# Kernel optimization log

Measured on AMD Instinct MI355X. Metric: run time of the kernel, lower is better.

## Reference

```python
import jax, jax.numpy as jnp
import numpy as np

HIDDEN = 1024
B, S = 4, 2048

def setup_inputs() -> dict:
    key = jax.random.key(0)
    k1, k2 = jax.random.split(key)
    hidden_states = jax.random.normal(k1, (B, S, HIDDEN), dtype=jnp.float32)
    # torch nn.Linear weight layout: [out_features, in_features]
    W_proj = jax.random.normal(k2, (3 * HIDDEN, HIDDEN), dtype=jnp.float32) * (1.0 / np.sqrt(HIDDEN))
    b_proj = jnp.zeros((3 * HIDDEN,), dtype=jnp.float32)
    return {"hidden_states": hidden_states, "W_proj": W_proj, "b_proj": b_proj}

def reference(hidden_states, W_proj, b_proj):
    h = hidden_states.shape[-1]
    # fused QKV projection: y = x @ W^T + b
    qkv = jnp.einsum('bsh,oh->bso', hidden_states, W_proj) + b_proj
    q, k, v = jnp.split(qkv, 3, axis=-1)  # each [B,S,H]
    scale = 1.0 / jnp.sqrt(jnp.asarray(h, dtype=q.dtype))
    scores = jnp.einsum('bqh,bkh->bqk', q, k) * scale  # [B,S,S]
    attn = jax.nn.softmax(scores, axis=-1)
    out = jnp.einsum('bqk,bkh->bqh', attn, v)
    return out
```

## Files before the change

### kernel.cpp

```cpp
#include <hip/hip_runtime.h>
#include <stdint.h>

#define HIDDEN 1024
#define BATCH  4
#define SEQ    2048
#define TOKENS (BATCH * SEQ)
#define QKVD   (3 * HIDDEN)

typedef unsigned short u16;
typedef __attribute__((ext_vector_type(8))) short   short8;
typedef __attribute__((ext_vector_type(4))) float   floatx4;

__device__ __forceinline__ u16 f32_bf16_rne(float f) {
    unsigned int u = __float_as_uint(f);
    u += 0x7FFFu + ((u >> 16) & 1u);
    return (u16)(u >> 16);
}

#define BAR() asm volatile("s_waitcnt lgkmcnt(0)\n\ts_barrier" ::: "memory")

__global__ __launch_bounds__(256) void cvt_bf16_kernel(
        const float* __restrict__ src, u16* __restrict__ dst, int n4) {
    int i = blockIdx.x * 256 + threadIdx.x;
    if (i >= n4) return;
    float4 v = ((const float4*)src)[i];
    ushort4 o;
    o.x = f32_bf16_rne(v.x); o.y = f32_bf16_rne(v.y);
    o.z = f32_bf16_rne(v.z); o.w = f32_bf16_rne(v.w);
    ((ushort4*)dst)[i] = o;
}

struct Stage { uint4 a0, a1, b0, b1; };

template <int EPI>
__global__ __launch_bounds__(256, 3) void gemm_bt(
        const u16* __restrict__ A, const u16* __restrict__ B,
        void* __restrict__ Cv, const float* __restrict__ bias,
        int K, int lda, int ldb, int ldc,
        size_t sA, size_t sB, size_t sC, float scale) {
    __shared__ u16 As0[4096], As1[4096];
    __shared__ u16 Bs0[4096], Bs1[4096];

    const int t    = threadIdx.x;
    const int lane = t & 63;
    const int wid  = t >> 6;
    const int bm   = blockIdx.y * 128;
    const int bn   = blockIdx.x * 128;

    const u16* Ab = A + (size_t)blockIdx.z * sA;
    const u16* Bb = B + (size_t)blockIdx.z * sB;

    const int srow = lane >> 2;
    const int scol = ((lane & 3) ^ ((lane >> 3) & 3)) * 8;

    const int wm = (wid >> 1) * 64;
    const int wn = (wid & 1) * 64;
    const int fr = lane & 15;
    const int fc = lane >> 4;
    const int foff = fr * 32 + ((fc ^ ((fr >> 1) & 3)) * 8);

    const int c0 = wid * 2, c1 = wid * 2 + 1;
    const u16* gA0 = Ab + (size_t)(bm + c0 * 16 + srow) * lda + scol;
    const u16* gA1 = Ab + (size_t)(bm + c1 * 16 + srow) * lda + scol;
    const u16* gB0 = Bb + (size_t)(bn + c0 * 16 + srow) * ldb + scol;
    const u16* gB1 = Bb + (size_t)(bn + c1 * 16 + srow) * ldb + scol;

    const int nk = K >> 5;

    auto ldst = [&](int kt) -> Stage {
        Stage s;
        const int off = kt << 5;
        s.a0 = *(const uint4*)(gA0 + off);
        s.a1 = *(const uint4*)(gA1 + off);
        s.b0 = *(const uint4*)(gB0 + off);
        s.b1 = *(const uint4*)(gB1 + off);
        return s;
    };
    auto wst = [&](u16* As_, u16* Bs_, const Stage& s) {
        *(uint4*)&As_[c0 * 512 + lane * 8] = s.a0;
        *(uint4*)&As_[c1 * 512 + lane * 8] = s.a1;
        *(uint4*)&Bs_[c0 * 512 + lane * 8] = s.b0;
        *(uint4*)&Bs_[c1 * 512 + lane * 8] = s.b1;
    };

    floatx4 acc[4][4];
#pragma unroll
    for (int i = 0; i < 4; i++)
#pragma unroll
        for (int j = 0; j < 4; j++) acc[i][j] = (floatx4){0.f, 0.f, 0.f, 0.f};

    auto compute = [&](const u16* As_, const u16* Bs_) {
        short8 bfr[4];
#pragma unroll
        for (int ni = 0; ni < 4; ni++)
            bfr[ni] = *(const short8*)&Bs_[((wn >> 4) + ni) * 512 + foff];
#pragma unroll
        for (int mi = 0; mi < 4; mi++) {
            short8 a = *(const short8*)&As_[((wm >> 4) + mi) * 512 + foff];
#pragma unroll
            for (int ni = 0; ni < 4; ni++)
                acc[mi][ni] = __builtin_amdgcn_mfma_f32_16x16x32_bf16(
                    a, bfr[ni], acc[mi][ni], 0, 0, 0);
        }
    };

    Stage ra = ldst(0);
    Stage rb = ldst(nk > 1 ? 1 : 0);
    wst(As0, Bs0, ra);
    BAR();

    for (int kt = 0; kt < nk; kt += 2) {
        ra = ldst(kt + 2 < nk ? kt + 2 : nk - 1);
        compute(As0, Bs0);
        wst(As1, Bs1, rb);
        BAR();
        rb = ldst(kt + 3 < nk ? kt + 3 : nk - 1);
        compute(As1, Bs1);
        wst(As0, Bs0, ra);
        BAR();
    }

    const int crow0 = bm + wm + (lane >> 4) * 4;
    const int ccol0 = bn + wn + fr;
    const size_t coff = (size_t)blockIdx.z * sC;

    if (EPI == 0) {
        u16* C = (u16*)Cv;
        float bv[4];
#pragma unroll
        for (int ni = 0; ni < 4; ni++) bv[ni] = bias[ccol0 + ni * 16];
#pragma unroll
        for (int mi = 0; mi < 4; mi++)
#pragma unroll
            for (int ni = 0; ni < 4; ni++)
#pragma unroll
                for (int r = 0; r < 4; r++)
                    C[coff + (size_t)(crow0 + mi * 16 + r) * ldc + (ccol0 + ni * 16)] =
                        f32_bf16_rne(acc[mi][ni][r] + bv[ni]);
    } else {
        float* C = (float*)Cv;
#pragma unroll
        for (int mi = 0; mi < 4; mi++)
#pragma unroll
            for (int ni = 0; ni < 4; ni++)
#pragma unroll
                for (int r = 0; r < 4; r++) {
                    float v = acc[mi][ni][r];
                    if (EPI == 1) v *= scale;
                    C[coff + (size_t)(crow0 + mi * 16 + r) * ldc + (ccol0 + ni * 16)] = v;
                }
    }
}

__global__ __launch_bounds__(256) void softmax_kernel(
        const float* __restrict__ S, u16* __restrict__ P) {
    __shared__ float redm[4];
    __shared__ float reds[4];
    const size_t base = (size_t)blockIdx.x * SEQ;
    const int t = threadIdx.x, lane = t & 63, wid = t >> 6;
    const float4* src = (const float4*)(S + base);
    float4 a = src[t], b = src[t + 256];

    float m = fmaxf(fmaxf(fmaxf(a.x, a.y), fmaxf(a.z, a.w)),
                    fmaxf(fmaxf(b.x, b.y), fmaxf(b.z, b.w)));
#pragma unroll
    for (int off = 32; off; off >>= 1) m = fmaxf(m, __shfl_xor(m, off, 64));
    if (lane == 0) redm[wid] = m;
    __syncthreads();
    m = fmaxf(fmaxf(redm[0], redm[1]), fmaxf(redm[2], redm[3]));

    float e[8];
    e[0] = __expf(a.x - m); e[1] = __expf(a.y - m);
    e[2] = __expf(a.z - m); e[3] = __expf(a.w - m);
    e[4] = __expf(b.x - m); e[5] = __expf(b.y - m);
    e[6] = __expf(b.z - m); e[7] = __expf(b.w - m);
    float s = e[0] + e[1] + e[2] + e[3] + e[4] + e[5] + e[6] + e[7];
#pragma unroll
    for (int off = 32; off; off >>= 1) s += __shfl_xor(s, off, 64);
    if (lane == 0) reds[wid] = s;
    __syncthreads();
    s = reds[0] + reds[1] + reds[2] + reds[3];
    const float r = 1.f / s;

    ushort4* dst = (ushort4*)(P + base);
    ushort4 o0, o1;
    o0.x = f32_bf16_rne(e[0] * r); o0.y = f32_bf16_rne(e[1] * r);
    o0.z = f32_bf16_rne(e[2] * r); o0.w = f32_bf16_rne(e[3] * r);
    o1.x = f32_bf16_rne(e[4] * r); o1.y = f32_bf16_rne(e[5] * r);
    o1.z = f32_bf16_rne(e[6] * r); o1.w = f32_bf16_rne(e[7] * r);
    dst[t] = o0;
    dst[t + 256] = o1;
}

__global__ __launch_bounds__(256) void transposeV_kernel(
        const u16* __restrict__ qkv, u16* __restrict__ Vt) {
    __shared__ u16 tile[64][66];
    const int b = blockIdx.z;
    const int s0 = blockIdx.x * 64, h0 = blockIdx.y * 64;
    const int t = threadIdx.x;
    const int c = t & 63, r4 = t >> 6;
#pragma unroll
    for (int i = 0; i < 16; i++) {
        int sl = i * 4 + r4;
        tile[sl][c] = qkv[(size_t)(b * SEQ + s0 + sl) * QKVD + 2 * HIDDEN + h0 + c];
    }
    __syncthreads();
#pragma unroll
    for (int i = 0; i < 16; i++) {
        int hl = i * 4 + r4;
        Vt[(size_t)(b * HIDDEN + h0 + hl) * SEQ + s0 + c] = tile[c][hl];
    }
}

extern "C" void kernel_launch(void* const* d_in, const int* in_sizes, int n_in,
                              void* d_out, int out_size, void* d_ws, size_t ws_size,
                              hipStream_t stream) {
    const float* x    = (const float*)d_in[0];
    const float* W    = (const float*)d_in[1];
    const float* bias = (const float*)d_in[2];
    float* out = (float*)d_out;

    u16* Xb  = (u16*)d_ws;
    u16* Wb  = Xb + (size_t)TOKENS * HIDDEN;
    u16* qkv = Wb + (size_t)QKVD * HIDDEN;
    float* scores = (float*)(qkv + (size_t)TOKENS * QKVD);
    u16* P  = (u16*)(scores + (size_t)BATCH * SEQ * SEQ);
    u16* Vt = P + (size_t)BATCH * SEQ * SEQ;

    cvt_bf16_kernel<<<TOKENS * HIDDEN / 4 / 256, 256, 0, stream>>>(x, Xb, TOKENS * HIDDEN / 4);
    cvt_bf16_kernel<<<QKVD * HIDDEN / 4 / 256, 256, 0, stream>>>(W, Wb, QKVD * HIDDEN / 4);

    gemm_bt<0><<<dim3(QKVD / 128, TOKENS / 128, 1), 256, 0, stream>>>(
        Xb, Wb, qkv, bias, HIDDEN, HIDDEN, HIDDEN, QKVD, 0, 0, 0, 1.f);

    gemm_bt<1><<<dim3(SEQ / 128, SEQ / 128, BATCH), 256, 0, stream>>>(
        qkv, qkv + HIDDEN, scores, nullptr, HIDDEN, QKVD, QKVD, SEQ,
        (size_t)SEQ * QKVD, (size_t)SEQ * QKVD, (size_t)SEQ * SEQ, 0.03125f);

    softmax_kernel<<<BATCH * SEQ, 256, 0, stream>>>(scores, P);

    transposeV_kernel<<<dim3(SEQ / 64, HIDDEN / 64, BATCH), 256, 0, stream>>>(qkv, Vt);

    gemm_bt<2><<<dim3(HIDDEN / 128, SEQ / 128, BATCH), 256, 0, stream>>>(
        P, Vt, out, nullptr, SEQ, SEQ, SEQ, HIDDEN,
        (size_t)SEQ * SEQ, (size_t)HIDDEN * SEQ, (size_t)SEQ * HIDDEN, 1.f);
}
```

Measured before the change: 275.3 us.

## Add 128x256 wide-tile GEMM for QKV and score GEMMs, merge conversion launches

New measurement: 679.0 us. 147% more time.

```diff
diff --git a/kernel.cpp b/kernel.cpp
--- a/kernel.cpp
+++ b/kernel.cpp
@@ -20,14 +20,138 @@
 #define BAR() asm volatile("s_waitcnt lgkmcnt(0)\n\ts_barrier" ::: "memory")
 
 __global__ __launch_bounds__(256) void cvt_bf16_kernel(
-        const float* __restrict__ src, u16* __restrict__ dst, int n4) {
+        const float* __restrict__ x, u16* __restrict__ xb,
+        const float* __restrict__ w, u16* __restrict__ wb,
+        int nx4, int nw4) {
     int i = blockIdx.x * 256 + threadIdx.x;
-    if (i >= n4) return;
+    const float* src; u16* dst;
+    if (i < nx4) { src = x; dst = xb; }
+    else { i -= nx4; if (i >= nw4) return; src = w; dst = wb; }
     float4 v = ((const float4*)src)[i];
     ushort4 o;
     o.x = f32_bf16_rne(v.x); o.y = f32_bf16_rne(v.y);
     o.z = f32_bf16_rne(v.z); o.w = f32_bf16_rne(v.w);
     ((ushort4*)dst)[i] = o;
+}
+
+struct StageW { uint4 v[6]; };
+
+template <int EPI>
+__global__ __launch_bounds__(256, 2) void gemm_bt_wide(
+        const u16* __restrict__ A, const u16* __restrict__ B,
+        void* __restrict__ Cv, const float* __restrict__ bias,
+        int K, int lda, int ldb, int ldc,
+        size_t sA, size_t sB, size_t sC, float scale) {
+    __shared__ u16 S0[12288], S1[12288];
+
+    const int t    = threadIdx.x;
+    const int lane = t & 63;
+    const int wid  = t >> 6;
+    const int bm   = blockIdx.y * 128;
+    const int bn   = blockIdx.x * 256;
+
+    const u16* Ab = A + (size_t)blockIdx.z * sA;
+    const u16* Bb = B + (size_t)blockIdx.z * sB;
+
+    const int srow = lane >> 2;
+    const int scol = ((lane & 3) ^ ((lane >> 3) & 3)) * 8;
+
+    const int wm = (wid >> 1) * 64;
+    const int wn = (wid & 1) * 128;
+    const int fr = lane & 15;
+    const int fc = lane >> 4;
+    const int foff = fr * 32 + ((fc ^ ((fr >> 1) & 3)) * 8);
+
+    const u16* gp[6];
+#pragma unroll
+    for (int j = 0; j < 6; j++) {
+        const int chunk = wid * 6 + j;
+        gp[j] = (chunk < 8)
+            ? Ab + (size_t)(bm + chunk * 16 + srow) * lda + scol
+            : Bb + (size_t)(bn + (chunk - 8) * 16 + srow) * ldb + scol;
+    }
+    const int lbase = (wid * 6) * 512 + lane * 8;
+
+    const int nk = K >> 5;
+
+    auto ldst = [&](int kt) -> StageW {
+        StageW s;
+        const int off = kt << 5;
+#pragma unroll
+        for (int j = 0; j < 6; j++) s.v[j] = *(const uint4*)(gp[j] + off);
+        return s;
+    };
+    auto wst = [&](u16* S_, const StageW& s) {
+#pragma unroll
+        for (int j = 0; j < 6; j++) *(uint4*)&S_[lbase + j * 512] = s.v[j];
+    };
+
+    floatx4 acc[8][4];
+#pragma unroll
+    for (int i = 0; i < 8; i++)
+#pragma unroll
+        for (int j = 0; j < 4; j++) acc[i][j] = (floatx4){0.f, 0.f, 0.f, 0.f};
+
+    auto compute = [&](const u16* S_) {
+        const u16* As_ = S_;
+        const u16* Bs_ = S_ + 4096;
+        short8 af[4];
+#pragma unroll
+        for (int mi = 0; mi < 4; mi++)
+            af[mi] = *(const short8*)&As_[((wm >> 4) + mi) * 512 + foff];
+#pragma unroll
+        for (int ni = 0; ni < 8; ni++) {
+            short8 bf = *(const short8*)&Bs_[((wn >> 4) + ni) * 512 + foff];
+#pragma unroll
+            for (int mi = 0; mi < 4; mi++)
+                acc[ni][mi] = __builtin_amdgcn_mfma_f32_16x16x32_bf16(
+                    af[mi], bf, acc[ni][mi], 0, 0, 0);
+        }
+    };
+
+    StageW ra = ldst(0);
+    StageW rb = ldst(nk > 1 ? 1 : 0);
+    wst(S0, ra);
+    BAR();
+
+    for (int kt = 0; kt < nk; kt += 2) {
+        ra = ldst(kt + 2 < nk ? kt + 2 : nk - 1);
+        compute(S0);
+        wst(S1, rb);
+        BAR();
+        rb = ldst(kt + 3 < nk ? kt + 3 : nk - 1);
+        compute(S1);
+        wst(S0, ra);
+        BAR();
+    }
+
+    const int crow0 = bm + wm + (lane >> 4) * 4;
+    const int ccol0 = bn + wn + fr;
+    const size_t coff = (size_t)blockIdx.z * sC;
+
+    if (EPI == 0) {
+        u16* C = (u16*)Cv;
+#pragma unroll
+        for (int ni = 0; ni < 8; ni++) {
+            const float bv = bias[ccol0 + ni * 16];
+#pragma unroll
+            for (int mi = 0; mi < 4; mi++)
+#pragma unroll
+                for (int r = 0; r < 4; r++)
+                    C[coff + (size_t)(crow0 + mi * 16 + r) * ldc + (ccol0 + ni * 16)] =
+                        f32_bf16_rne(acc[ni][mi][r] + bv);
+        }
+    } else {
+        float* C = (float*)Cv;
+#pragma unroll
+        for (int ni = 0; ni < 8; ni++)
+#pragma unroll
+            for (int mi = 0; mi < 4; mi++)
+#pragma unroll
+                for (int r = 0; r < 4; r++)
+                    C[coff + (size_t)(crow0 + mi * 16 + r) * ldc + (ccol0 + ni * 16)] =
+                        acc[ni][mi][r] * scale;
+    }
 }
 
 struct Stage { uint4 a0, a1, b0, b1; };
@@ -124,32 +248,17 @@
     const int ccol0 = bn + wn + fr;
     const size_t coff = (size_t)blockIdx.z * sC;
 
-    if (EPI == 0) {
-        u16* C = (u16*)Cv;
-        float bv[4];
-#pragma unroll
-        for (int ni = 0; ni < 4; ni++) bv[ni] = bias[ccol0 + ni * 16];
-#pragma unroll
-        for (int mi = 0; mi < 4; mi++)
-#pragma unroll
-            for (int ni = 0; ni < 4; ni++)
-#pragma unroll
-                for (int r = 0; r < 4; r++)
-                    C[coff + (size_t)(crow0 + mi * 16 + r) * ldc + (ccol0 + ni * 16)] =
-                        f32_bf16_rne(acc[mi][ni][r] + bv[ni]);
-    } else {
-        float* C = (float*)Cv;
-#pragma unroll
-        for (int mi = 0; mi < 4; mi++)
-#pragma unroll
-            for (int ni = 0; ni < 4; ni++)
-#pragma unroll
-                for (int r = 0; r < 4; r++) {
-                    float v = acc[mi][ni][r];
-                    if (EPI == 1) v *= scale;
-                    C[coff + (size_t)(crow0 + mi * 16 + r) * ldc + (ccol0 + ni * 16)] = v;
-                }
-    }
+    float* C = (float*)Cv;
+#pragma unroll
+    for (int mi = 0; mi < 4; mi++)
+#pragma unroll
+        for (int ni = 0; ni < 4; ni++)
+#pragma unroll
+            for (int r = 0; r < 4; r++) {
+                float v = acc[mi][ni][r];
+                if (EPI == 1) v *= scale;
+                C[coff + (size_t)(crow0 + mi * 16 + r) * ldc + (ccol0 + ni * 16)] = v;
+            }
 }
 
 __global__ __launch_bounds__(256) void softmax_kernel(
@@ -227,13 +336,13 @@
     u16* P  = (u16*)(scores + (size_t)BATCH * SEQ * SEQ);
     u16* Vt = P + (size_t)BATCH * SEQ * SEQ;
 
-    cvt_bf16_kernel<<<TOKENS * HIDDEN / 4 / 256, 256, 0, stream>>>(x, Xb, TOKENS * HIDDEN / 4);
-    cvt_bf16_kernel<<<QKVD * HIDDEN / 4 / 256, 256, 0, stream>>>(W, Wb, QKVD * HIDDEN / 4);
-
-    gemm_bt<0><<<dim3(QKVD / 128, TOKENS / 128, 1), 256, 0, stream>>>(
+    const int nx4 = TOKENS * HIDDEN / 4, nw4 = QKVD * HIDDEN / 4;
+    cvt_bf16_kernel<<<(nx4 + nw4 + 255) / 256, 256, 0, stream>>>(x, Xb, W, Wb, nx4, nw4);
+
+    gemm_bt_wide<0><<<dim3(QKVD / 256, TOKENS / 128, 1), 256, 0, stream>>>(
         Xb, Wb, qkv, bias, HIDDEN, HIDDEN, HIDDEN, QKVD, 0, 0, 0, 1.f);
 
-    gemm_bt<1><<<dim3(SEQ / 128, SEQ / 128, BATCH), 256, 0, stream>>>(
+    gemm_bt_wide<1><<<dim3(SEQ / 256, SEQ / 128, BATCH), 256, 0, stream>>>(
         qkv, qkv + HIDDEN, scores, nullptr, HIDDEN, QKVD, QKVD, SEQ,
         (size_t)SEQ * QKVD, (size_t)SEQ * QKVD, (size_t)SEQ * SEQ, 0.03125f);
 
```

## Load GEMM A fragments directly from global memory and merge conversion kernels

Applied to the files above, without the earlier changes.

New measurement: 378.8 us. 1.38x slower.

```diff
diff --git a/kernel.cpp b/kernel.cpp
--- a/kernel.cpp
+++ b/kernel.cpp
@@ -20,9 +20,13 @@
 #define BAR() asm volatile("s_waitcnt lgkmcnt(0)\n\ts_barrier" ::: "memory")
 
 __global__ __launch_bounds__(256) void cvt_bf16_kernel(
-        const float* __restrict__ src, u16* __restrict__ dst, int n4) {
+        const float* __restrict__ x, u16* __restrict__ xb,
+        const float* __restrict__ w, u16* __restrict__ wb,
+        int nx4, int nw4) {
     int i = blockIdx.x * 256 + threadIdx.x;
-    if (i >= n4) return;
+    const float* src; u16* dst;
+    if (i < nx4) { src = x; dst = xb; }
+    else { i -= nx4; if (i >= nw4) return; src = w; dst = wb; }
     float4 v = ((const float4*)src)[i];
     ushort4 o;
     o.x = f32_bf16_rne(v.x); o.y = f32_bf16_rne(v.y);
@@ -30,15 +34,14 @@
     ((ushort4*)dst)[i] = o;
 }
 
-struct Stage { uint4 a0, a1, b0, b1; };
+struct StageB { uint4 b0, b1; };
 
 template <int EPI>
-__global__ __launch_bounds__(256, 3) void gemm_bt(
+__global__ __launch_bounds__(256, 3) void gemm_adirect(
         const u16* __restrict__ A, const u16* __restrict__ B,
         void* __restrict__ Cv, const float* __restrict__ bias,
         int K, int lda, int ldb, int ldc,
         size_t sA, size_t sB, size_t sC, float scale) {
-    __shared__ u16 As0[4096], As1[4096];
     __shared__ u16 Bs0[4096], Bs1[4096];
 
     const int t    = threadIdx.x;
@@ -52,36 +55,44 @@
 
     const int srow = lane >> 2;
     const int scol = ((lane & 3) ^ ((lane >> 3) & 3)) * 8;
+    const int c0 = wid * 2, c1 = wid * 2 + 1;
+    const u16* gB0 = Bb + (size_t)(bn + c0 * 16 + srow) * ldb + scol;
+    const u16* gB1 = Bb + (size_t)(bn + c1 * 16 + srow) * ldb + scol;
 
     const int wm = (wid >> 1) * 64;
     const int wn = (wid & 1) * 64;
     const int fr = lane & 15;
     const int fc = lane >> 4;
+    const int fk = fc * 8;
     const int foff = fr * 32 + ((fc ^ ((fr >> 1) & 3)) * 8);
 
-    const int c0 = wid * 2, c1 = wid * 2 + 1;
-    const u16* gA0 = Ab + (size_t)(bm + c0 * 16 + srow) * lda + scol;
-    const u16* gA1 = Ab + (size_t)(bm + c1 * 16 + srow) * lda + scol;
-    const u16* gB0 = Bb + (size_t)(bn + c0 * 16 + srow) * ldb + scol;
-    const u16* gB1 = Bb + (size_t)(bn + c1 * 16 + srow) * ldb + scol;
+    const u16* gA[4];
+#pragma unroll
+    for (int mi = 0; mi < 4; mi++)
+        gA[mi] = Ab + (size_t)(bm + wm + mi * 16 + fr) * lda + fk;
 
     const int nk = K >> 5;
 
-    auto ldst = [&](int kt) -> Stage {
-        Stage s;
+    auto ldB = [&](int kt) -> StageB {
+        StageB s;
         const int off = kt << 5;
-        s.a0 = *(const uint4*)(gA0 + off);
-        s.a1 = *(const uint4*)(gA1 + off);
         s.b0 = *(const uint4*)(gB0 + off);
         s.b1 = *(const uint4*)(gB1 + off);
         return s;
     };
-    auto wst = [&](u16* As_, u16* Bs_, const Stage& s) {
-        *(uint4*)&As_[c0 * 512 + lane * 8] = s.a0;
-        *(uint4*)&As_[c1 * 512 + lane * 8] = s.a1;
+    auto wstB = [&](u16* Bs_, const StageB& s) {
         *(uint4*)&Bs_[c0 * 512 + lane * 8] = s.b0;
         *(uint4*)&Bs_[c1 * 512 + lane * 8] = s.b1;
     };
+    struct AFrag { short8 f[4]; };
+    auto ldA = [&](int kt) -> AFrag {
+        AFrag a;
+        const int off = kt << 5;
+#pragma unroll
+        for (int mi = 0; mi < 4; mi++)
+            a.f[mi] = *(const short8*)(gA[mi] + off);
+        return a;
+    };
 
     floatx4 acc[4][4];
 #pragma unroll
@@ -89,34 +100,35 @@
 #pragma unroll
         for (int j = 0; j < 4; j++) acc[i][j] = (floatx4){0.f, 0.f, 0.f, 0.f};
 
-    auto compute = [&](const u16* As_, const u16* Bs_) {
+    auto compute = [&](const u16* Bs_, const AFrag& a) {
         short8 bfr[4];
 #pragma unroll
         for (int ni = 0; ni < 4; ni++)
             bfr[ni] = *(const short8*)&Bs_[((wn >> 4) + ni) * 512 + foff];
 #pragma unroll
-        for (int mi = 0; mi < 4; mi++) {
-            short8 a = *(const short8*)&As_[((wm >> 4) + mi) * 512 + foff];
+        for (int mi = 0; mi < 4; mi++)
 #pragma unroll
             for (int ni = 0; ni < 4; ni++)
                 acc[mi][ni] = __builtin_amdgcn_mfma_f32_16x16x32_bf16(
-                    a, bfr[ni], acc[mi][ni], 0, 0, 0);
-        }
-    };
-
-    Stage ra = ldst(0);
-    Stage rb = ldst(nk > 1 ? 1 : 0);
-    wst(As0, Bs0, ra);
+                    a.f[mi], bfr[ni], acc[mi][ni], 0, 0, 0);
+    };
+
+    StageB rb = ldB(0);
+    wstB(Bs0, rb);
+    rb = ldB(nk > 1 ? 1 : 0);
+    AFrag fa = ldA(0);
     BAR();
 
     for (int kt = 0; kt < nk; kt += 2) {
-        ra = ldst(kt + 2 < nk ? kt + 2 : nk - 1);
-        compute(As0, Bs0);
-        wst(As1, Bs1, rb);
+        AFrag fa2 = ldA(kt + 1 < nk ? kt + 1 : 0);
+        compute(Bs0, fa);
+        wstB(Bs1, rb);
+        rb = ldB(kt + 2 < nk ? kt + 2 : 0);
         BAR();
-        rb = ldst(kt + 3 < nk ? kt + 3 : nk - 1);
-        compute(As1, Bs1);
-        wst(As0, Bs0, ra);
+        fa = ldA(kt + 2 < nk ? kt + 2 : 0);
+        compute(Bs1, fa2);
+        wstB(Bs0, rb);
+        rb = ldB(kt + 3 < nk ? kt + 3 : 0);
         BAR();
     }
 
@@ -126,17 +138,16 @@
 
     if (EPI == 0) {
         u16* C = (u16*)Cv;
-        float bv[4];
-#pragma unroll
-        for (int ni = 0; ni < 4; ni++) bv[ni] = bias[ccol0 + ni * 16];
-#pragma unroll
-        for (int mi = 0; mi < 4; mi++)
-#pragma unroll
-            for (int ni = 0; ni < 4; ni++)
+#pragma unroll
+        for (int ni = 0; ni < 4; ni++) {
+            const float bv = bias[ccol0 + ni * 16];
+#pragma unroll
+            for (int mi = 0; mi < 4; mi++)
 #pragma unroll
                 for (int r = 0; r < 4; r++)
                     C[coff + (size_t)(crow0 + mi * 16 + r) * ldc + (ccol0 + ni * 16)] =
-                        f32_bf16_rne(acc[mi][ni][r] + bv[ni]);
+                        f32_bf16_rne(acc[mi][ni][r] + bv);
+        }
     } else {
         float* C = (float*)Cv;
 #pragma unroll
@@ -227,13 +238,13 @@
     u16* P  = (u16*)(scores + (size_t)BATCH * SEQ * SEQ);
     u16* Vt = P + (size_t)BATCH * SEQ * SEQ;
 
-    cvt_bf16_kernel<<<TOKENS * HIDDEN / 4 / 256, 256, 0, stream>>>(x, Xb, TOKENS * HIDDEN / 4);
-    cvt_bf16_kernel<<<QKVD * HIDDEN / 4 / 256, 256, 0, stream>>>(W, Wb, QKVD * HIDDEN / 4);
-
-    gemm_bt<0><<<dim3(QKVD / 128, TOKENS / 128, 1), 256, 0, stream>>>(
+    const int nx4 = TOKENS * HIDDEN / 4, nw4 = QKVD * HIDDEN / 4;
+    cvt_bf16_kernel<<<(nx4 + nw4 + 255) / 256, 256, 0, stream>>>(x, Xb, W, Wb, nx4, nw4);
+
+    gemm_adirect<0><<<dim3(QKVD / 128, TOKENS / 128, 1), 256, 0, stream>>>(
         Xb, Wb, qkv, bias, HIDDEN, HIDDEN, HIDDEN, QKVD, 0, 0, 0, 1.f);
 
-    gemm_bt<1><<<dim3(SEQ / 128, SEQ / 128, BATCH), 256, 0, stream>>>(
+    gemm_adirect<1><<<dim3(SEQ / 128, SEQ / 128, BATCH), 256, 0, stream>>>(
         qkv, qkv + HIDDEN, scores, nullptr, HIDDEN, QKVD, QKVD, SEQ,
         (size_t)SEQ * QKVD, (size_t)SEQ * QKVD, (size_t)SEQ * SEQ, 0.03125f);
 
@@ -241,7 +252,7 @@
 
     transposeV_kernel<<<dim3(SEQ / 64, HIDDEN / 64, BATCH), 256, 0, stream>>>(qkv, Vt);
 
-    gemm_bt<2><<<dim3(HIDDEN / 128, SEQ / 128, BATCH), 256, 0, stream>>>(
+    gemm_adirect<2><<<dim3(HIDDEN / 128, SEQ / 128, BATCH), 256, 0, stream>>>(
         P, Vt, out, nullptr, SEQ, SEQ, SEQ, HIDDEN,
         (size_t)SEQ * SEQ, (size_t)HIDDEN * SEQ, (size_t)SEQ * HIDDEN, 1.f);
 }
```
